# Optimization experiments

Measured on AMD Instinct MI355X. Metric: run time of the kernel, lower is better.

Reference implementation:

```python
import jax, jax.numpy as jnp
import numpy as np

N = 4096      # num utterances (graph nodes)
D = 512       # utt_embed_size * 2
W = 10        # att_window_size
S = 8         # num speakers
WIN = 2 * W + 1


def setup_inputs() -> dict:
    key = jax.random.key(0)
    ks = jax.random.split(key, 7)
    s = 0.05  # keep activations in a sane range through two layers
    return {
        "context_embeds": jax.random.normal(ks[0], (N, D), jnp.float32),
        "speakers": jax.random.randint(ks[1], (N,), 0, S),
        "w_gc1": jax.random.normal(ks[2], (4, D, D), jnp.float32) * s,
        "w_gc2": jax.random.normal(ks[3], (4, D, D), jnp.float32) * s,
        "w_att": jax.random.normal(ks[4], (D, D), jnp.float32) * s,
        "w_aggr1": jax.random.normal(ks[5], (D, D), jnp.float32) * s,
        "w_aggr2": jax.random.normal(ks[6], (D, D), jnp.float32) * s,
    }


def _relation_adjs(x, speakers, w_att):
    """Windowed edge attention + 4 relation-masked adjacency matrices."""
    n = x.shape[0]
    pad = jnp.zeros((W, D), x.dtype)
    padded = jnp.concatenate([pad, x, pad], axis=0)          # [n+2W, D]
    # banded gather: row j sees padded[j : j+2W+1]  == cols j-W .. j+W
    gidx = jnp.arange(n)[:, None] + jnp.arange(WIN)[None, :]
    fat = padded[gidx]
    raw = jnp.einsum('nwd,ed->nwe', fat, w_att)               # Linear: x @ W^T
    scores = jnp.einsum('nwe,ne->nw', raw, x)
    attn = jax.nn.softmax(scores, axis=1)                     # softmax over full window (pads included, as original)
    # scatter attention into a banded [n, n] mask
    cols = jnp.arange(n)[:, None] + jnp.arange(WIN)[None, :] - W
    valid = (cols >= 0) & (cols < n)
    rows = jnp.broadcast_to(jnp.arange(n)[:, None], cols.shape)
    attn_mask = jnp.zeros((n, n), x.dtype).at[
        rows, jnp.clip(cols, 0, n - 1)].add(jnp.where(valid, attn, 0.0))
    i = jnp.arange(n)[:, None]
    j = jnp.arange(n)[None, :]
    band = jnp.abs(j - i) <= W
    same_spk = speakers[:, None] == speakers[None, :]
    pred = ((j >= i) & band).astype(x.dtype) * attn_mask      # successors-in-time kept (triu) within window
    suc = ((j < i) & band).astype(x.dtype) * attn_mask        # strict past within window
    same = (same_spk & band).astype(x.dtype) * attn_mask
    diff = ((~same_spk) & band).astype(x.dtype) * attn_mask
    return jnp.stack([pred, suc, same, diff])                 # [4, n, n]


def _gcn_layer(h, adjs, w_gc, w_aggr):
    # sum_r  A_r @ (h @ W_r)  + h @ W_aggr, then relu
    hw = jnp.einsum('md,rde->rme', h, w_gc)                   # [4, n, D]
    agg = jnp.einsum('rnm,rme->ne', adjs, hw)                 # [n, D]
    return jax.nn.relu(agg + h @ w_aggr)


def reference(context_embeds, speakers, w_gc1, w_gc2, w_att, w_aggr1, w_aggr2):
    adjs = _relation_adjs(context_embeds, speakers, w_att)
    h1 = _gcn_layer(context_embeds, adjs, w_gc1, w_aggr1)
    h2 = _gcn_layer(h1, adjs, w_gc2, w_aggr2)
    return h2
```

## Files before the change

### kernel.cpp

```cpp
#include <hip/hip_runtime.h>


#define NN 4096

typedef __bf16 bf16x8 __attribute__((ext_vector_type(8)));
typedef float f32x4 __attribute__((ext_vector_type(4)));
typedef unsigned short u16;
typedef unsigned int u32;

__device__ __forceinline__ u16 f2bf(float f) {
  unsigned u = __float_as_uint(f);
  unsigned r = u + 0x7FFFu + ((u >> 16) & 1u);
  return (u16)(r >> 16);
}
__device__ __forceinline__ float bf2f(u16 h) {
  return __uint_as_float(((unsigned)h) << 16);
}
__device__ __forceinline__ float blo(u32 v) { return __uint_as_float(v << 16); }
__device__ __forceinline__ float bhi(u32 v) { return __uint_as_float(v & 0xffff0000u); }
__device__ __forceinline__ u32 packbf(float a, float b) {
  return (u32)f2bf(a) | ((u32)f2bf(b) << 16);
}

__device__ __forceinline__ void gload_lds16(const u16* g, u16* l) {
  __builtin_amdgcn_global_load_lds(
      (const __attribute__((address_space(1))) void*)g,
      (__attribute__((address_space(3))) void*)l, 16, 0, 0);
}

__global__ void prep_all(const float* __restrict__ x, const float* __restrict__ w_att,
                         const float* __restrict__ w_gc1, const float* __restrict__ w_aggr1,
                         const float* __restrict__ w_gc2, const float* __restrict__ w_aggr2,
                         const int* __restrict__ spk,
                         u16* __restrict__ Aatt, u16* __restrict__ Batt,
                         u16* __restrict__ Wt1, u16* __restrict__ Wt2,
                         float* __restrict__ xp, u32* __restrict__ xWg,
                         u32* __restrict__ h1Wg, int* __restrict__ spkp) {
  const int b = blockIdx.x, tid = threadIdx.x;
  if (b < 8192) {
    int idx = b * 256 + tid;
    int r = idx >> 9, c = idx & 511;
    float v = x[idx];
    u16 hi = f2bf(v), lo = f2bf(v - bf2f(hi));
    u16* row = Aatt + (size_t)r * 1536;
    row[c] = hi; row[512 + c] = lo; row[1024 + c] = hi;
    xp[(size_t)(r + 16) * 512 + c] = v;
  } else if (b < 9216) {
    int idx = (b - 8192) * 256 + tid;
    int j = idx >> 9, e = idx & 511;
    float v = w_att[(size_t)e * 512 + j];
    u16 hi = f2bf(v), lo = f2bf(v - bf2f(hi));
    u16* row = Batt + (size_t)j * 1536;
    row[e] = hi; row[512 + e] = hi; row[1024 + e] = lo;
  } else if (b < 17408) {
    int lay = (b >= 13312);
    int idx = (b - (lay ? 13312 : 9216)) * 256 + tid;
    const float* g = lay ? w_gc2 : w_gc1;
    const float* wa = lay ? w_aggr2 : w_aggr1;
    u16* Wt = lay ? Wt2 : Wt1;
    int j = idx >> 9, k = idx & 511;
    int p = j >> 9, jj = j & 511;
    size_t o = (size_t)k * 512 + jj;
    float v;
    if (p == 0)      v = g[o] - g[262144 + o];
    else if (p == 1) v = g[524288 + o] - g[786432 + o];
    else if (p == 2) v = g[262144 + o] + g[786432 + o];
    else             v = wa[o];
    Wt[(size_t)j * 512 + k] = f2bf(v);
  } else if (b < 17472) {
    int idx = (b - 17408) * 256 + tid;
    int g = idx >> 9, c = idx & 511;
    int row = (g < 16) ? g : 4112 + (g - 16);
    xp[(size_t)row * 512 + c] = 0.f;
  } else if (b < 17600) {
    int idx = (b - 17472) * 256 + tid;
    int g = idx >> 10, c = idx & 1023;
    int row = (g < 16) ? g : 4112 + (g - 16);
    xWg[(size_t)row * 1024 + c] = 0;
  } else if (b < 17728) {
    int idx = (b - 17600) * 256 + tid;
    int g = idx >> 10, c = idx & 1023;
    int row = (g < 16) ? g : 4112 + (g - 16);
    h1Wg[(size_t)row * 1024 + c] = 0;
  } else {
    int idx = (b - 17728) * 256 + tid;
    if (idx < 4128)
      spkp[idx] = (idx >= 16 && idx < 4112) ? spk[idx - 16] : -9;
  }
}

__device__ __forceinline__ void xcd_swz(int gx, int& bx, int& by) {
  int lid = by * gx + bx;
  int cpx = (gx * (int)gridDim.y) >> 3;
  int nl = (lid & 7) * cpx + (lid >> 3);
  by = nl / gx;
  bx = nl - by * gx;
}

__device__ __forceinline__ void gemm_core(const u16* __restrict__ A, const u16* __restrict__ Bt,
                                          int K, int lda, int ldb, size_t bm, size_t bn,
                                          u16 (&As)[2][8192], u16 (&Bs)[2][8192],
                                          f32x4 (&acc)[4][4]) {
  const int tid = threadIdx.x;
  const int lane = tid & 63;
  const int wave = tid >> 6;
  const int wr = wave >> 1, wc = wave & 1;
  const int arow = wr * 64 + (lane & 15);
  const int bcol = wc * 64 + (lane & 15);
  const int nt = K >> 6;

  auto STAGE = [&](int t, int bi) {
    const int k0 = t << 6;
#pragma unroll
    for (int c4 = 0; c4 < 4; ++c4) {
      const int o = (c4 * 256 + tid) * 16;
      const int r = o >> 7;
      const int sc = (((o >> 4) & 7) ^ (r & 7)) << 3;
      gload_lds16(A + (bm + r) * lda + k0 + sc, &As[bi][o >> 1]);
      gload_lds16(Bt + (bn + r) * ldb + k0 + sc, &Bs[bi][o >> 1]);
    }
  };

  STAGE(0, 0);
  for (int t = 0; t < nt; ++t) {
    const int cur = t & 1;
    if (t + 1 < nt) {
      STAGE(t + 1, cur ^ 1);
      asm volatile("s_waitcnt vmcnt(8)" ::: "memory");
    } else {
      asm volatile("s_waitcnt vmcnt(0)" ::: "memory");
    }
    __builtin_amdgcn_s_barrier();
    asm volatile("" ::: "memory");
    bf16x8 af[4][2], bfr[4][2];
#pragma unroll
    for (int i = 0; i < 4; ++i)
#pragma unroll
      for (int ks = 0; ks < 2; ++ks) {
        const int ar = arow + i * 16;
        const int ac = ((ks * 4 + (lane >> 4)) ^ (ar & 7)) << 4;
        af[i][ks] = *(const bf16x8*)((const char*)&As[cur][0] + ar * 128 + ac);
        const int br = bcol + i * 16;
        const int bc = ((ks * 4 + (lane >> 4)) ^ (br & 7)) << 4;
        bfr[i][ks] = *(const bf16x8*)((const char*)&Bs[cur][0] + br * 128 + bc);
      }
#pragma unroll
    for (int ks = 0; ks < 2; ++ks)
#pragma unroll
      for (int i = 0; i < 4; ++i)
#pragma unroll
        for (int j = 0; j < 4; ++j)
          acc[i][j] = __builtin_amdgcn_mfma_f32_16x16x32_bf16(af[i][ks], bfr[j][ks],
                                                              acc[i][j], 0, 0, 0);
    asm volatile("s_waitcnt lgkmcnt(0)" ::: "memory");
    __builtin_amdgcn_sched_barrier(0);
    __builtin_amdgcn_s_barrier();
  }
}

__global__ __launch_bounds__(256, 2) void fat_gemm(const u16* __restrict__ Aatt,
                                                   const u16* __restrict__ Wt1,
                                                   const u16* __restrict__ Batt,
                                                   u16* __restrict__ xW, float* __restrict__ y) {
  __shared__ u16 As[2][8192];
  __shared__ u16 Bs[2][8192];
  f32x4 acc[4][4] = {};
  const int tid = threadIdx.x;
  const int lane = tid & 63;
  const int wave = tid >> 6;
  const int wr = wave >> 1, wc = wave & 1;
  int bx = blockIdx.x, by = blockIdx.y;
  xcd_swz(20, bx, by);
  const size_t bm = (size_t)by * 128;
  const bool yp = bx < 4;
  const size_t bn = yp ? (size_t)bx * 128 : (size_t)(bx - 4) * 128;

  if (yp)
    gemm_core(Aatt, Batt, 1536, 1536, 1536, bm, bn, As, Bs, acc);
  else
    gemm_core(Aatt, Wt1, 512, 1536, 512, bm, bn, As, Bs, acc);

  const size_t crow = bm + wr * 64 + ((lane >> 4) * 4);
  const size_t ccol = bn + wc * 64 + (lane & 15);
#pragma unroll
  for (int i = 0; i < 4; ++i)
#pragma unroll
    for (int j = 0; j < 4; ++j)
#pragma unroll
      for (int b = 0; b < 4; ++b) {
        size_t r = crow + i * 16 + b, c = ccol + j * 16;
        if (yp)
          y[r * 512 + c] = acc[i][j][b];
        else
          xW[r * 2048 + c] = f2bf(acc[i][j][b]);
      }
}

__global__ __launch_bounds__(256, 2) void gemm_l2(const u16* __restrict__ h1,
                                                  const u16* __restrict__ Wt2,
                                                  u16* __restrict__ h1W) {
  __shared__ u16 As[2][8192];
  __shared__ u16 Bs[2][8192];
  f32x4 acc[4][4] = {};
  const int tid = threadIdx.x;
  const int lane = tid & 63;
  const int wave = tid >> 6;
  const int wr = wave >> 1, wc = wave & 1;
  int bx = blockIdx.x, by = blockIdx.y;
  xcd_swz(16, bx, by);
  const size_t bm = (size_t)by * 128;
  const size_t bn = (size_t)bx * 128;
  gemm_core(h1, Wt2, 512, 512, 512, bm, bn, As, Bs, acc);
  const size_t crow = bm + wr * 64 + ((lane >> 4) * 4);
  const size_t ccol = bn + wc * 64 + (lane & 15);
#pragma unroll
  for (int i = 0; i < 4; ++i)
#pragma unroll
    for (int j = 0; j < 4; ++j)
#pragma unroll
      for (int b = 0; b < 4; ++b) {
        size_t r = crow + i * 16 + b, c = ccol + j * 16;
        h1W[r * 2048 + c] = f2bf(acc[i][j][b]);
      }
}

__device__ __forceinline__ int xcd_row(int b) { return (b & 7) * 512 + (b >> 3); }

__global__ void scores_k(const float* __restrict__ xp, const float* __restrict__ y,
                         float* __restrict__ attn) {
  const int n = xcd_row(blockIdx.x);
  const int tid = threadIdx.x;
  __shared__ float ys[512];
  __shared__ float sc[21];
  ys[tid] = y[(size_t)n * 512 + tid];
  ys[tid + 256] = y[(size_t)n * 512 + tid + 256];
  __syncthreads();
  const int wave = tid >> 6, lane = tid & 63;
  for (int w = wave; w < 21; w += 4) {
    const float* xm = xp + (size_t)(n + 6 + w) * 512;
    float p = 0.f;
#pragma unroll
    for (int i = 0; i < 8; ++i) p += xm[lane + i * 64] * ys[lane + i * 64];
#pragma unroll
    for (int off = 32; off; off >>= 1) p += __shfl_xor(p, off, 64);
    if (lane == 0) sc[w] = p;
  }
  __syncthreads();
  if (tid < 64) {
    float v = (tid < 21) ? sc[tid] : -1e30f;
    float mx = v;
#pragma unroll
    for (int off = 32; off; off >>= 1) mx = fmaxf(mx, __shfl_xor(mx, off, 64));
    float e = (tid < 21) ? __expf(v - mx) : 0.f;
    float sum = e;
#pragma unroll
    for (int off = 32; off; off >>= 1) sum += __shfl_xor(sum, off, 64);
    if (tid < 21) {
      int m = n + tid - 10;
      attn[(size_t)n * 24 + tid] = (0 <= m && m < NN) ? (e / sum) : 0.f;
    }
  }
}

template <int OUT_BF16>
__global__ __launch_bounds__(256) void bandagg(const u32* __restrict__ P32,
                                               const float* __restrict__ attn,
                                               const int* __restrict__ spkp,
                                               void* __restrict__ out) {
  const int b = blockIdx.x;
  const int n0 = (((b & 7) << 6) + (b >> 3)) << 3;
  const int tid = threadIdx.x;
  const int* spk16 = spkp + 16;

  int msp[8];
#pragma unroll
  for (int r = 0; r < 8; ++r) msp[r] = spk16[n0 + r];

  float accL[8], accH[8];
#pragma unroll
  for (int r = 0; r < 8; ++r) {
    u32 sv = P32[(size_t)(n0 + r) * 1024 + 768 + tid];
    accL[r] = blo(sv);
    accH[r] = bhi(sv);
  }

#pragma unroll
  for (int j = 0; j < 28; ++j) {
    const ptrdiff_t mrow = (ptrdiff_t)(n0 - 10 + j) * 1024;
    u32 vp = P32[mrow + tid];
    u32 vs = P32[mrow + 256 + tid];
    u32 va = P32[mrow + 512 + tid];
    float pl = blo(vp), ph = bhi(vp);
    float sl = blo(vs), sh = bhi(vs);
    float al = blo(va), ah = bhi(va);
    const int mspk = spk16[n0 - 10 + j];
#pragma unroll
    for (int r = 0; r < 8; ++r) {
      const int w = j - r;
      if (w < 0 || w > 20) continue;
      float a = attn[(size_t)(n0 + r) * 24 + w];
      float as = (mspk == msp[r]) ? a : 0.f;
      accL[r] += a * al;
      accH[r] += a * ah;
      accL[r] += as * sl;
      accH[r] += as * sh;
      if (w >= 10) {
        accL[r] += a * pl;
        accH[r] += a * ph;
      }
    }
  }

#pragma unroll
  for (int r = 0; r < 8; ++r) {
    float lo = fmaxf(accL[r], 0.f), hi = fmaxf(accH[r], 0.f);
    if (OUT_BF16) {
      ((u32*)out)[(size_t)(n0 + r) * 256 + tid] = packbf(lo, hi);
    } else {
      float2 v = {lo, hi};
      ((float2*)out)[(size_t)(n0 + r) * 256 + tid] = v;
    }
  }
}

extern "C" void kernel_launch(void* const* d_in, const int* in_sizes, int n_in,
                              void* d_out, int out_size, void* d_ws, size_t ws_size,
                              hipStream_t stream) {
  const float* x = (const float*)d_in[0];
  const int* spk = (const int*)d_in[1];
  const float* w_gc1 = (const float*)d_in[2];
  const float* w_gc2 = (const float*)d_in[3];
  const float* w_att = (const float*)d_in[4];
  const float* w_aggr1 = (const float*)d_in[5];
  const float* w_aggr2 = (const float*)d_in[6];

  char* p = (char*)d_ws;
  u16* Aatt = (u16*)p;  p += (size_t)NN * 1536 * 2;
  u16* Batt = (u16*)p;  p += (size_t)512 * 1536 * 2;
  u16* Wt1 = (u16*)p;   p += (size_t)2048 * 512 * 2;
  u16* Wt2 = (u16*)p;   p += (size_t)2048 * 512 * 2;
  float* xp = (float*)p; p += (size_t)4128 * 512 * 4;
  float* y = (float*)p; p += (size_t)NN * 512 * 4;
  float* attn = (float*)p; p += (size_t)NN * 24 * 4;
  u16* xWg = (u16*)p;   p += (size_t)4128 * 2048 * 2;
  u16* h1 = (u16*)p;    p += (size_t)NN * 512 * 2;
  u16* h1Wg = (u16*)p;  p += (size_t)4128 * 2048 * 2;
  int* spkp = (int*)p;  p += (size_t)4128 * 4;

  u16* xW = xWg + (size_t)16 * 2048;
  u16* h1W = h1Wg + (size_t)16 * 2048;

  prep_all<<<17745, 256, 0, stream>>>(x, w_att, w_gc1, w_aggr1, w_gc2, w_aggr2, spk,
                                      Aatt, Batt, Wt1, Wt2, xp, (u32*)xWg, (u32*)h1Wg,
                                      spkp);

  fat_gemm<<<dim3(20, 32), 256, 0, stream>>>(Aatt, Wt1, Batt, xW, y);

  scores_k<<<NN, 256, 0, stream>>>(xp, y, attn);

  bandagg<1><<<512, 256, 0, stream>>>((const u32*)xW, attn, spkp, h1);

  gemm_l2<<<dim3(16, 32), 256, 0, stream>>>(h1, Wt2, h1W);

  bandagg<0><<<512, 256, 0, stream>>>((const u32*)h1W, attn, spkp, d_out);
}
```

Baseline: 104.2 us.

## Fuse attention score/softmax kernel into first band-aggregation kernel

Removes the separate scores_k launch and computes the windowed attention scores and softmax inside the first bandagg kernel for its 8 rows, writing attn for reuse by the second layer. The aggregation is restructured to preload all 28 neighbour rows into registers and stage attention and speaker ids in shared memory, and launch bounds now request two blocks per CU. This saves one launch and a global round-trip of attn, but only 512 blocks now do the score dot products (previously 4096), which lowers parallelism in that phase and raises register pressure.

After: 106.2 us. No clear change (+1.9%).

```diff
diff --git a/kernel.cpp b/kernel.cpp
--- a/kernel.cpp
+++ b/kernel.cpp
@@ -224,101 +224,100 @@
       }
 }
 
-__device__ __forceinline__ int xcd_row(int b) { return (b & 7) * 512 + (b >> 3); }
-
-__global__ void scores_k(const float* __restrict__ xp, const float* __restrict__ y,
-                         float* __restrict__ attn) {
-  const int n = xcd_row(blockIdx.x);
-  const int tid = threadIdx.x;
-  __shared__ float ys[512];
-  __shared__ float sc[21];
-  ys[tid] = y[(size_t)n * 512 + tid];
-  ys[tid + 256] = y[(size_t)n * 512 + tid + 256];
-  __syncthreads();
-  const int wave = tid >> 6, lane = tid & 63;
-  for (int w = wave; w < 21; w += 4) {
-    const float* xm = xp + (size_t)(n + 6 + w) * 512;
-    float p = 0.f;
-#pragma unroll
-    for (int i = 0; i < 8; ++i) p += xm[lane + i * 64] * ys[lane + i * 64];
-#pragma unroll
-    for (int off = 32; off; off >>= 1) p += __shfl_xor(p, off, 64);
-    if (lane == 0) sc[w] = p;
-  }
-  __syncthreads();
-  if (tid < 64) {
-    float v = (tid < 21) ? sc[tid] : -1e30f;
-    float mx = v;
-#pragma unroll
-    for (int off = 32; off; off >>= 1) mx = fmaxf(mx, __shfl_xor(mx, off, 64));
-    float e = (tid < 21) ? __expf(v - mx) : 0.f;
-    float sum = e;
-#pragma unroll
-    for (int off = 32; off; off >>= 1) sum += __shfl_xor(sum, off, 64);
-    if (tid < 21) {
-      int m = n + tid - 10;
-      attn[(size_t)n * 24 + tid] = (0 <= m && m < NN) ? (e / sum) : 0.f;
-    }
-  }
-}
-
-template <int OUT_BF16>
-__global__ __launch_bounds__(256) void bandagg(const u32* __restrict__ P32,
-                                               const float* __restrict__ attn,
-                                               const int* __restrict__ spkp,
-                                               void* __restrict__ out) {
+template <int PH>
+__global__ __launch_bounds__(256, 2) void bandagg(const u32* __restrict__ P32,
+                                                  const float* __restrict__ xp,
+                                                  const float* __restrict__ y,
+                                                  float* __restrict__ attn,
+                                                  const int* __restrict__ spkp,
+                                                  void* __restrict__ out) {
   const int b = blockIdx.x;
   const int n0 = (((b & 7) << 6) + (b >> 3)) << 3;
   const int tid = threadIdx.x;
-  const int* spk16 = spkp + 16;
-
-  int msp[8];
-#pragma unroll
-  for (int r = 0; r < 8; ++r) msp[r] = spk16[n0 + r];
-
-  float accL[8], accH[8];
+  __shared__ float at[8][24];
+  __shared__ int spb[28];
+  __shared__ float ys[8][512];
+
+  if (tid < 28) spb[tid] = spkp[16 + n0 - 10 + tid];
+  if (PH == 1) {
+    for (int i = tid; i < 4096; i += 256)
+      ys[i >> 9][i & 511] = y[(size_t)(n0 + (i >> 9)) * 512 + (i & 511)];
+  } else {
+    if (tid < 192) at[tid / 24][tid % 24] = attn[(size_t)(n0 + tid / 24) * 24 + tid % 24];
+  }
+  __syncthreads();
+
+  if (PH == 1) {
+    const int wv = tid >> 6, lane = tid & 63;
+    for (int rr = wv; rr < 8; rr += 4) {
+      const int n = n0 + rr;
+      for (int w = 0; w < 21; ++w) {
+        const float* xm = xp + (size_t)(n + 6 + w) * 512;
+        float p = 0.f;
+#pragma unroll
+        for (int i = 0; i < 8; ++i) p += xm[lane + i * 64] * ys[rr][lane + i * 64];
+#pragma unroll
+        for (int off = 32; off; off >>= 1) p += __shfl_xor(p, off, 64);
+        if (lane == 0) at[rr][w] = p;
+      }
+      float v = (lane < 21) ? at[rr][lane] : -1e30f;
+      float mx = v;
+#pragma unroll
+      for (int off = 32; off; off >>= 1) mx = fmaxf(mx, __shfl_xor(mx, off, 64));
+      float e = (lane < 21) ? __expf(v - mx) : 0.f;
+      float sum = e;
+#pragma unroll
+      for (int off = 32; off; off >>= 1) sum += __shfl_xor(sum, off, 64);
+      if (lane < 21) {
+        int m = n + lane - 10;
+        float a = (0 <= m && m < NN) ? (e / sum) : 0.f;
+        at[rr][lane] = a;
+        attn[(size_t)n * 24 + lane] = a;
+      }
+    }
+    __syncthreads();
+  }
+
+  const int c = tid;
+  u32 vP[28], vS[28], vA[28];
+#pragma unroll
+  for (int j = 0; j < 28; ++j) {
+    const u32* rowp = P32 + (ptrdiff_t)(n0 - 10 + j) * 1024 + c;
+    vP[j] = rowp[0];
+    vS[j] = rowp[256];
+    vA[j] = rowp[512];
+  }
+  int sb[28];
+#pragma unroll
+  for (int j = 0; j < 28; ++j) sb[j] = spb[j];
+
 #pragma unroll
   for (int r = 0; r < 8; ++r) {
-    u32 sv = P32[(size_t)(n0 + r) * 1024 + 768 + tid];
-    accL[r] = blo(sv);
-    accH[r] = bhi(sv);
-  }
-
-#pragma unroll
-  for (int j = 0; j < 28; ++j) {
-    const ptrdiff_t mrow = (ptrdiff_t)(n0 - 10 + j) * 1024;
-    u32 vp = P32[mrow + tid];
-    u32 vs = P32[mrow + 256 + tid];
-    u32 va = P32[mrow + 512 + tid];
-    float pl = blo(vp), ph = bhi(vp);
-    float sl = blo(vs), sh = bhi(vs);
-    float al = blo(va), ah = bhi(va);
-    const int mspk = spk16[n0 - 10 + j];
-#pragma unroll
-    for (int r = 0; r < 8; ++r) {
-      const int w = j - r;
-      if (w < 0 || w > 20) continue;
-      float a = attn[(size_t)(n0 + r) * 24 + w];
-      float as = (mspk == msp[r]) ? a : 0.f;
-      accL[r] += a * al;
-      accH[r] += a * ah;
-      accL[r] += as * sl;
-      accH[r] += as * sh;
+    float wv_[21];
+#pragma unroll
+    for (int w = 0; w < 21; ++w) wv_[w] = at[r][w];
+    const int s0 = sb[10 + r];
+    u32 sv = P32[(size_t)(n0 + r) * 1024 + 768 + c];
+    float aL = blo(sv), aH = bhi(sv);
+#pragma unroll
+    for (int w = 0; w < 21; ++w) {
+      const int j = r + w;
+      const float a = wv_[w];
+      const float as = (sb[j] == s0) ? a : 0.f;
+      aL += a * blo(vA[j]) + as * blo(vS[j]);
+      aH += a * bhi(vA[j]) + as * bhi(vS[j]);
       if (w >= 10) {
-        accL[r] += a * pl;
-        accH[r] += a * ph;
-      }
-    }
-  }
-
-#pragma unroll
-  for (int r = 0; r < 8; ++r) {
-    float lo = fmaxf(accL[r], 0.f), hi = fmaxf(accH[r], 0.f);
-    if (OUT_BF16) {
-      ((u32*)out)[(size_t)(n0 + r) * 256 + tid] = packbf(lo, hi);
+        aL += a * blo(vP[j]);
+        aH += a * bhi(vP[j]);
+      }
+    }
+    aL = fmaxf(aL, 0.f);
+    aH = fmaxf(aH, 0.f);
+    if (PH == 1) {
+      ((u32*)out)[(size_t)(n0 + r) * 256 + c] = packbf(aL, aH);
     } else {
-      float2 v = {lo, hi};
-      ((float2*)out)[(size_t)(n0 + r) * 256 + tid] = v;
+      float2 o = {aL, aH};
+      ((float2*)out)[(size_t)(n0 + r) * 256 + c] = o;
     }
   }
 }
@@ -356,11 +355,9 @@
 
   fat_gemm<<<dim3(20, 32), 256, 0, stream>>>(Aatt, Wt1, Batt, xW, y);
 
-  scores_k<<<NN, 256, 0, stream>>>(xp, y, attn);
-
-  bandagg<1><<<512, 256, 0, stream>>>((const u32*)xW, attn, spkp, h1);
+  bandagg<1><<<512, 256, 0, stream>>>((const u32*)xW, xp, y, attn, spkp, h1);
 
   gemm_l2<<<dim3(16, 32), 256, 0, stream>>>(h1, Wt2, h1W);
 
-  bandagg<0><<<512, 256, 0, stream>>>((const u32*)h1W, attn, spkp, d_out);
-}
+  bandagg<2><<<512, 256, 0, stream>>>((const u32*)h1W, xp, y, attn, spkp, d_out);
+}
```

## Fuse attention scores into band aggregation with one block per row

Applied to the files above, without the earlier changes.

Merges the score/softmax kernel into the first band-aggregation pass, which removes one launch and the attention round-trip before its first use. The aggregation is also reorganised: each row now gets its own block, and each of the four waves handles one relation slice (pred, same-speaker, all, self) with 16-byte vector loads. The per-wave partials are then reduced through shared memory. This gives up the old 8-row register reuse of neighbour rows across outputs, so each neighbour row is reloaded about 21 times through cache, and it adds an LDS reduction plus extra syncs.

Result: slower. 111.5 us (+7.0%).

```diff
diff --git a/kernel.cpp b/kernel.cpp
--- a/kernel.cpp
+++ b/kernel.cpp
@@ -226,100 +226,104 @@
 
 __device__ __forceinline__ int xcd_row(int b) { return (b & 7) * 512 + (b >> 3); }
 
-__global__ void scores_k(const float* __restrict__ xp, const float* __restrict__ y,
-                         float* __restrict__ attn) {
+template <int PH>
+__global__ __launch_bounds__(256) void gatherP(const u32* __restrict__ P32,
+                                               const float* __restrict__ xp,
+                                               const float* __restrict__ y,
+                                               float* __restrict__ attn,
+                                               const int* __restrict__ spkp,
+                                               void* __restrict__ out) {
   const int n = xcd_row(blockIdx.x);
-  const int tid = threadIdx.x;
+  const int tid = threadIdx.x, lane = tid & 63, wv = tid >> 6;
+  __shared__ float av[21], apv[21], asv[21];
+  __shared__ float sc[21];
+  __shared__ int sps[21];
+  __shared__ float red[4][512];
   __shared__ float ys[512];
-  __shared__ float sc[21];
-  ys[tid] = y[(size_t)n * 512 + tid];
-  ys[tid + 256] = y[(size_t)n * 512 + tid + 256];
-  __syncthreads();
-  const int wave = tid >> 6, lane = tid & 63;
-  for (int w = wave; w < 21; w += 4) {
-    const float* xm = xp + (size_t)(n + 6 + w) * 512;
-    float p = 0.f;
-#pragma unroll
-    for (int i = 0; i < 8; ++i) p += xm[lane + i * 64] * ys[lane + i * 64];
-#pragma unroll
-    for (int off = 32; off; off >>= 1) p += __shfl_xor(p, off, 64);
-    if (lane == 0) sc[w] = p;
-  }
-  __syncthreads();
-  if (tid < 64) {
-    float v = (tid < 21) ? sc[tid] : -1e30f;
-    float mx = v;
-#pragma unroll
-    for (int off = 32; off; off >>= 1) mx = fmaxf(mx, __shfl_xor(mx, off, 64));
-    float e = (tid < 21) ? __expf(v - mx) : 0.f;
-    float sum = e;
-#pragma unroll
-    for (int off = 32; off; off >>= 1) sum += __shfl_xor(sum, off, 64);
+
+  const int mysp = spkp[16 + n];
+  if (tid < 21) sps[tid] = spkp[16 + n - 10 + tid];
+
+  if (PH == 1) {
+    ys[tid] = y[(size_t)n * 512 + tid];
+    ys[tid + 256] = y[(size_t)n * 512 + tid + 256];
+    __syncthreads();
+    for (int w = wv; w < 21; w += 4) {
+      const float* xm = xp + (size_t)(n + 6 + w) * 512;
+      float p = 0.f;
+#pragma unroll
+      for (int i = 0; i < 8; ++i) p += xm[lane + i * 64] * ys[lane + i * 64];
+#pragma unroll
+      for (int off = 32; off; off >>= 1) p += __shfl_xor(p, off, 64);
+      if (lane == 0) sc[w] = p;
+    }
+    __syncthreads();
+    if (tid < 64) {
+      float v = (tid < 21) ? sc[tid] : -1e30f;
+      float mx = v;
+#pragma unroll
+      for (int off = 32; off; off >>= 1) mx = fmaxf(mx, __shfl_xor(mx, off, 64));
+      float e = (tid < 21) ? __expf(v - mx) : 0.f;
+      float sum = e;
+#pragma unroll
+      for (int off = 32; off; off >>= 1) sum += __shfl_xor(sum, off, 64);
+      if (tid < 21) {
+        int m = n + tid - 10;
+        float a = (0 <= m && m < NN) ? (e / sum) : 0.f;
+        av[tid] = a;
+        apv[tid] = (tid >= 10) ? a : 0.f;
+        asv[tid] = (sps[tid] == mysp) ? a : 0.f;
+        attn[(size_t)n * 24 + tid] = a;
+      }
+    }
+    __syncthreads();
+  } else {
     if (tid < 21) {
       int m = n + tid - 10;
-      attn[(size_t)n * 24 + tid] = (0 <= m && m < NN) ? (e / sum) : 0.f;
-    }
-  }
-}
-
-template <int OUT_BF16>
-__global__ __launch_bounds__(256) void bandagg(const u32* __restrict__ P32,
-                                               const float* __restrict__ attn,
-                                               const int* __restrict__ spkp,
-                                               void* __restrict__ out) {
-  const int b = blockIdx.x;
-  const int n0 = (((b & 7) << 6) + (b >> 3)) << 3;
-  const int tid = threadIdx.x;
-  const int* spk16 = spkp + 16;
-
-  int msp[8];
-#pragma unroll
-  for (int r = 0; r < 8; ++r) msp[r] = spk16[n0 + r];
-
-  float accL[8], accH[8];
-#pragma unroll
-  for (int r = 0; r < 8; ++r) {
-    u32 sv = P32[(size_t)(n0 + r) * 1024 + 768 + tid];
-    accL[r] = blo(sv);
-    accH[r] = bhi(sv);
-  }
-
-#pragma unroll
-  for (int j = 0; j < 28; ++j) {
-    const ptrdiff_t mrow = (ptrdiff_t)(n0 - 10 + j) * 1024;
-    u32 vp = P32[mrow + tid];
-    u32 vs = P32[mrow + 256 + tid];
-    u32 va = P32[mrow + 512 + tid];
-    float pl = blo(vp), ph = bhi(vp);
-    float sl = blo(vs), sh = bhi(vs);
-    float al = blo(va), ah = bhi(va);
-    const int mspk = spk16[n0 - 10 + j];
-#pragma unroll
-    for (int r = 0; r < 8; ++r) {
-      const int w = j - r;
-      if (w < 0 || w > 20) continue;
-      float a = attn[(size_t)(n0 + r) * 24 + w];
-      float as = (mspk == msp[r]) ? a : 0.f;
-      accL[r] += a * al;
-      accH[r] += a * ah;
-      accL[r] += as * sl;
-      accH[r] += as * sh;
-      if (w >= 10) {
-        accL[r] += a * pl;
-        accH[r] += a * ph;
-      }
-    }
-  }
-
-#pragma unroll
-  for (int r = 0; r < 8; ++r) {
-    float lo = fmaxf(accL[r], 0.f), hi = fmaxf(accH[r], 0.f);
-    if (OUT_BF16) {
-      ((u32*)out)[(size_t)(n0 + r) * 256 + tid] = packbf(lo, hi);
-    } else {
-      float2 v = {lo, hi};
-      ((float2*)out)[(size_t)(n0 + r) * 256 + tid] = v;
-    }
+      float a = attn[(size_t)n * 24 + tid];
+      av[tid] = a;
+      apv[tid] = (tid >= 10) ? a : 0.f;
+      asv[tid] = (sps[tid] == mysp) ? a : 0.f;
+    }
+    __syncthreads();
+  }
+
+  const int pofs = (wv == 0) ? 0 : (wv == 1 ? 256 : 512);
+  const int wlo = (wv == 0) ? 10 : (wv == 3 ? 11 : 0);
+  const int whi = (wv == 2) ? 11 : 21;
+  const float* wgt = (wv == 0) ? apv : (wv == 1 ? asv : av);
+
+  float acc[8] = {};
+  for (int w = wlo; w < whi; ++w) {
+    const float a = wgt[w];
+    const uint4 v = *(const uint4*)(P32 + (ptrdiff_t)(n - 10 + w) * 1024 + pofs + lane * 4);
+    acc[0] += a * blo(v.x); acc[1] += a * bhi(v.x);
+    acc[2] += a * blo(v.y); acc[3] += a * bhi(v.y);
+    acc[4] += a * blo(v.z); acc[5] += a * bhi(v.z);
+    acc[6] += a * blo(v.w); acc[7] += a * bhi(v.w);
+  }
+  if (wv == 3) {
+    const uint4 v = *(const uint4*)(P32 + (size_t)n * 1024 + 768 + lane * 4);
+    acc[0] += blo(v.x); acc[1] += bhi(v.x);
+    acc[2] += blo(v.y); acc[3] += bhi(v.y);
+    acc[4] += blo(v.z); acc[5] += bhi(v.z);
+    acc[6] += blo(v.w); acc[7] += bhi(v.w);
+  }
+
+#pragma unroll
+  for (int k = 0; k < 8; ++k) red[wv][lane * 8 + k] = acc[k];
+  __syncthreads();
+
+  float s0 = red[0][2 * tid] + red[1][2 * tid] + red[2][2 * tid] + red[3][2 * tid];
+  float s1 = red[0][2 * tid + 1] + red[1][2 * tid + 1] + red[2][2 * tid + 1] +
+             red[3][2 * tid + 1];
+  s0 = fmaxf(s0, 0.f);
+  s1 = fmaxf(s1, 0.f);
+  if (PH == 1) {
+    ((u32*)out)[(size_t)n * 256 + tid] = packbf(s0, s1);
+  } else {
+    float2 o = {s0, s1};
+    ((float2*)out)[(size_t)n * 256 + tid] = o;
   }
 }
 
@@ -356,11 +360,9 @@
 
   fat_gemm<<<dim3(20, 32), 256, 0, stream>>>(Aatt, Wt1, Batt, xW, y);
 
-  scores_k<<<NN, 256, 0, stream>>>(xp, y, attn);
-
-  bandagg<1><<<512, 256, 0, stream>>>((const u32*)xW, attn, spkp, h1);
+  gatherP<1><<<NN, 256, 0, stream>>>((const u32*)xW, xp, y, attn, spkp, h1);
 
   gemm_l2<<<dim3(16, 32), 256, 0, stream>>>(h1, Wt2, h1W);
 
-  bandagg<0><<<512, 256, 0, stream>>>((const u32*)h1W, attn, spkp, d_out);
-}
+  gatherP<2><<<NN, 256, 0, stream>>>((const u32*)h1W, xp, y, attn, spkp, d_out);
+}
```
